# Optimization experiments

Measured on AMD Instinct MI355X. Metric: run time of the kernel, lower is better.

## Reference

```python
import jax, jax.numpy as jnp
import numpy as np

N = 50000; E = 1600000; F_IN = 32; HEADS = 8; D = 16; HID = HEADS * D
ED = 16; G = 512; MH = 512; MO = 512; SLOPE = 0.2


def setup_inputs() -> dict:
    key = jax.random.key(0)
    ks = jax.random.split(key, 40)
    inp = {}
    inp["x"] = jax.random.normal(ks[0], (N, F_IN), jnp.float32)
    inp["edge_index"] = jax.random.randint(ks[1], (2, E), 0, N)
    inp["edge_attr"] = jax.random.normal(ks[2], (E, ED), jnp.float32)
    inp["batch"] = jnp.sort(jax.random.randint(ks[3], (N,), 0, G))

    def lin(k, fi, fo):
        return jax.random.normal(k, (fi, fo), jnp.float32) / np.sqrt(fi).astype(np.float32)

    i = 4
    dims = [(F_IN, HID), (HID, HID), (HID, HID)]  # GATv2 layers 0..2
    for l, (fi, fo) in enumerate(dims):
        inp[f"Wl{l}"] = lin(ks[i], fi, fo); i += 1
        inp[f"bl{l}"] = jnp.zeros((fo,), jnp.float32)
        inp[f"Wr{l}"] = lin(ks[i], fi, fo); i += 1
        inp[f"br{l}"] = jnp.zeros((fo,), jnp.float32)
        inp[f"We{l}"] = lin(ks[i], ED, fo); i += 1
        inp[f"att{l}"] = jax.random.normal(ks[i], (HEADS, D), jnp.float32) / np.sqrt(D).astype(np.float32); i += 1
        inp[f"b{l}"] = jnp.zeros((fo,), jnp.float32)
    inp["mW1"] = lin(ks[i], HID, MH); i += 1
    inp["mb1"] = jnp.zeros((MH,), jnp.float32)
    inp["ln_g"] = jnp.ones((MH,), jnp.float32)
    inp["ln_b"] = jnp.zeros((MH,), jnp.float32)
    inp["mW2"] = lin(ks[i], MH, MO); i += 1
    inp["mb2"] = jnp.zeros((MO,), jnp.float32)
    return inp


def _gatv2(h, src, dst, ea, Wl, bl, Wr, br, We, att, b):
    # One GATv2Conv layer (eval mode, add_self_loops already applied).
    n = h.shape[0]
    xl = (h @ Wl + bl).reshape(n, HEADS, D)   # source transform
    xr = (h @ Wr + br).reshape(n, HEADS, D)   # target transform
    ee = (ea @ We).reshape(-1, HEADS, D)      # edge transform (no bias in PyG)
    m = xl[src] + xr[dst] + ee                # [E', H, D]
    m = jnp.where(m > 0, m, SLOPE * m)        # LeakyReLU(0.2)
    s = jnp.einsum('ehd,hd->eh', m, att)      # attention logits
    mx = jax.ops.segment_max(s, dst, num_segments=n)
    ex = jnp.exp(s - mx[dst])
    den = jax.ops.segment_sum(ex, dst, num_segments=n)
    alpha = ex / den[dst]                     # softmax over incoming edges
    out = jax.ops.segment_sum(alpha[:, :, None] * xl[src], dst, num_segments=n)
    return out.reshape(n, HEADS * D) + b


def _forward(x, edge_index, edge_attr, batch,
             Wl0, bl0, Wr0, br0, We0, att0, b0,
             Wl1, bl1, Wr1, br1, We1, att1, b1,
             Wl2, bl2, Wr2, br2, We2, att2, b2,
             mW1, mb1, ln_g, ln_b, mW2, mb2):
    src, dst = edge_index[0], edge_index[1]
    # add_self_loops with fill_value='mean': self-loop edge_attr = mean of incoming edge_attr
    cnt = jax.ops.segment_sum(jnp.ones((E,), jnp.float32), dst, num_segments=N)
    loop_attr = jax.ops.segment_sum(edge_attr, dst, num_segments=N) / jnp.clip(cnt, 1.0)[:, None]
    nodes = jnp.arange(N)
    src_f = jnp.concatenate([src, nodes])
    dst_f = jnp.concatenate([dst, nodes])
    ea = jnp.concatenate([edge_attr, loop_attr], axis=0)

    h = jax.nn.relu(_gatv2(x, src_f, dst_f, ea, Wl0, bl0, Wr0, br0, We0, att0, b0))
    h = jax.nn.relu(_gatv2(h, src_f, dst_f, ea, Wl1, bl1, Wr1, br1, We1, att1, b1))
    h = _gatv2(h, src_f, dst_f, ea, Wl2, bl2, Wr2, br2, We2, att2, b2)

    g = jax.ops.segment_sum(h, batch, num_segments=G)  # sum pooling per graph
    z = jax.nn.relu(g @ mW1 + mb1)
    mu = jnp.mean(z, axis=-1, keepdims=True)
    var = jnp.var(z, axis=-1, keepdims=True)
    z = (z - mu) / jnp.sqrt(var + 1e-5) * ln_g + ln_b
    return z @ mW2 + mb2


def reference(x, edge_index, edge_attr, batch,
              Wl0, bl0, Wr0, br0, We0, att0, b0,
              Wl1, bl1, Wr1, br1, We1, att1, b1,
              Wl2, bl2, Wr2, br2, We2, att2, b2,
              mW1, mb1, ln_g, ln_b, mW2, mb2):
    return _forward(x, edge_index, edge_attr, batch,
                    Wl0, bl0, Wr0, br0, We0, att0, b0,
                    Wl1, bl1, Wr1, br1, We1, att1, b1,
                    Wl2, bl2, Wr2, br2, We2, att2, b2,
                    mW1, mb1, ln_g, ln_b, mW2, mb2)
```

## Files before the change

### kernel.cpp

```cpp
#include <hip/hip_runtime.h>
#include <math.h>

#define NN 50000
#define EE 1600000
#define FIN 32
#define HID_ 128
#define ED_ 16
#define GG 512
#define MH_ 512
#define MO_ 512

#if __has_builtin(__builtin_amdgcn_exp2f)
#define EXP2(x) __builtin_amdgcn_exp2f(x)
#else
#define EXP2(x) exp2f(x)
#endif


__global__ void hist_kernel(const int* __restrict__ dst, int* __restrict__ cnt) {
  int e = blockIdx.x * 256 + threadIdx.x;
  if (e < EE) atomicAdd(&cnt[dst[e]], 1);
}

__global__ __launch_bounds__(256) void scan1_kernel(const int* __restrict__ in, int n,
                                                    int* __restrict__ out,
                                                    int* __restrict__ bsums) {
  int chunk = blockIdx.x;
  int base = chunk * 1024;
  int t = threadIdx.x;
  int idx = base + t * 4;
  int v0 = (idx + 0 < n) ? in[idx + 0] : 0;
  int v1 = (idx + 1 < n) ? in[idx + 1] : 0;
  int v2 = (idx + 2 < n) ? in[idx + 2] : 0;
  int v3 = (idx + 3 < n) ? in[idx + 3] : 0;
  int ts = v0 + v1 + v2 + v3;
  int lane = t & 63, w = t >> 6;
  int s = ts;
#pragma unroll
  for (int off = 1; off < 64; off <<= 1) {
    int o = __shfl_up(s, off);
    if (lane >= off) s += o;
  }
  __shared__ int wsum[4];
  if (lane == 63) wsum[w] = s;
  __syncthreads();
  int woff = 0;
  for (int i = 0; i < w; i++) woff += wsum[i];
  int excl = woff + s - ts;
  int run = excl;
  run += v0; if (idx + 0 < n) out[idx + 0] = run;
  run += v1; if (idx + 1 < n) out[idx + 1] = run;
  run += v2; if (idx + 2 < n) out[idx + 2] = run;
  run += v3; if (idx + 3 < n) out[idx + 3] = run;
  if (t == 255) bsums[chunk] = woff + s;
}

__global__ void scan_add_kernel(int* __restrict__ rowptr, const int* __restrict__ bscan, int n) {
  int i = blockIdx.x * 256 + threadIdx.x;
  if (i == 0) rowptr[0] = 0;
  if (i < n) {
    int chunk = i >> 10;
    if (chunk > 0) rowptr[1 + i] += bscan[chunk - 1];
  }
}

__global__ void scatter_kernel(const int* __restrict__ src, const int* __restrict__ dst,
                               const int* __restrict__ rowptr, int* __restrict__ fill,
                               int2* __restrict__ csr) {
  int e = blockIdx.x * 256 + threadIdx.x;
  if (e >= EE) return;
  int v = dst[e];
  int pos = rowptr[v] + atomicAdd(&fill[v], 1);
  csr[pos] = make_int2(src[e], e);
}

__global__ __launch_bounds__(256) void loopattr_kernel(const int* __restrict__ rowptr,
                                                       const int2* __restrict__ csr,
                                                       const float* __restrict__ ea,
                                                       float* __restrict__ la) {
  int wid = threadIdx.x >> 6, lane = threadIdx.x & 63;
  int v = __builtin_amdgcn_readfirstlane(blockIdx.x * 4 + wid);
  if (v >= NN) return;
  int s = __builtin_amdgcn_readfirstlane(rowptr[v]);
  int e = __builtin_amdgcn_readfirstlane(rowptr[v + 1]);
  int k = lane >> 4;
  int d = lane & 15;
  float acc = 0.f;
  for (int j = s + k; j < e; j += 4) acc += ea[(size_t)csr[j].y * 16 + d];
  acc += __shfl_xor(acc, 16);
  acc += __shfl_xor(acc, 32);
  if (lane < 16) la[(size_t)v * 16 + d] = (e > s) ? acc / (float)(e - s) : 0.f;
}


template <int F>
__global__ __launch_bounds__(256) void node_transform(const float* __restrict__ h,
                                                      const float* __restrict__ Wlm,
                                                      const float* __restrict__ blm,
                                                      const float* __restrict__ Wrm,
                                                      const float* __restrict__ brm,
                                                      float* __restrict__ xl,
                                                      float* __restrict__ xr, int nnodes) {
  __shared__ float hs[F * 32];
  int v0 = blockIdx.x * 32;
  int t = threadIdx.x;
  for (int idx = t; idx < 32 * F; idx += 256) {
    int i = idx / F, k = idx - i * F;
    float val = (v0 + i < nnodes) ? h[(size_t)(v0 + i) * F + k] : 0.f;
    hs[k * 32 + i] = val;
  }
  __syncthreads();
  int cc = t & 127;
  bool isL = t < 128;
  const float* W = isL ? Wlm : Wrm;
  float4 acc[8];
#pragma unroll
  for (int q = 0; q < 8; q++) acc[q] = make_float4(0.f, 0.f, 0.f, 0.f);
  const float4* hs4 = (const float4*)hs;
  for (int k = 0; k < F; k++) {
    float w = W[k * 128 + cc];
#pragma unroll
    for (int q = 0; q < 8; q++) {
      float4 hv = hs4[k * 8 + q];
      acc[q].x = fmaf(hv.x, w, acc[q].x);
      acc[q].y = fmaf(hv.y, w, acc[q].y);
      acc[q].z = fmaf(hv.z, w, acc[q].z);
      acc[q].w = fmaf(hv.w, w, acc[q].w);
    }
  }
  float b = isL ? blm[cc] : brm[cc];
  float* dstp = isL ? xl : xr;
  int nb = nnodes - v0; if (nb > 32) nb = 32;
#pragma unroll
  for (int q = 0; q < 8; q++) {
    if (4 * q + 0 < nb) dstp[(size_t)(v0 + 4 * q + 0) * 128 + cc] = acc[q].x + b;
    if (4 * q + 1 < nb) dstp[(size_t)(v0 + 4 * q + 1) * 128 + cc] = acc[q].y + b;
    if (4 * q + 2 < nb) dstp[(size_t)(v0 + 4 * q + 2) * 128 + cc] = acc[q].z + b;
    if (4 * q + 3 < nb) dstp[(size_t)(v0 + 4 * q + 3) * 128 + cc] = acc[q].w + b;
  }
}


__global__ __launch_bounds__(256) void gat_aggregate(
    const float* __restrict__ xl, const float* __restrict__ xr,
    const int* __restrict__ rowptr, const int2* __restrict__ csr,
    const float* __restrict__ ea, const float* __restrict__ la,
    const float* __restrict__ We, const float* __restrict__ att,
    const float* __restrict__ bias, float* __restrict__ hout, int relu) {
  int wid = threadIdx.x >> 6, lane = threadIdx.x & 63;
  int v = __builtin_amdgcn_readfirstlane(blockIdx.x * 4 + wid);
  if (v >= NN) return;
  int c0 = lane, c1 = 64 + lane;
  float wec0[16], wec1[16];
#pragma unroll
  for (int k = 0; k < 16; k++) {
    wec0[k] = We[k * 128 + c0];
    wec1[k] = We[k * 128 + c1];
  }
  const float L2E = 1.44269504088896340736f;
  float a0 = att[c0] * L2E, a1 = att[c1] * L2E;
  float xr0 = xr[(size_t)v * 128 + c0], xr1 = xr[(size_t)v * 128 + c1];

  auto score = [&](int u, const float* eaP,
                   float& xlu0, float& xlu1, float& p0, float& p1) {
    float ec[16];
#pragma unroll
    for (int k = 0; k < 4; k++) {
      float4 q = ((const float4*)eaP)[k];
      ec[4 * k + 0] = q.x; ec[4 * k + 1] = q.y;
      ec[4 * k + 2] = q.z; ec[4 * k + 3] = q.w;
    }
    const float* xlu = xl + (size_t)u * 128;
    xlu0 = xlu[c0]; xlu1 = xlu[c1];
    float m0 = xr0 + xlu0, m1 = xr1 + xlu1;
#pragma unroll
    for (int k = 0; k < 16; k++) {
      m0 = fmaf(ec[k], wec0[k], m0);
      m1 = fmaf(ec[k], wec1[k], m1);
    }
    m0 = fmaxf(m0, 0.2f * m0);
    m1 = fmaxf(m1, 0.2f * m1);
    p0 = a0 * m0; p1 = a1 * m1;
#pragma unroll
    for (int off = 1; off < 16; off <<= 1) {
      p0 += __shfl_xor(p0, off);
      p1 += __shfl_xor(p1, off);
    }
  };

  float mx0, mx1, den0 = 1.f, den1 = 1.f, acc0, acc1;
  {
    float xs0, xs1, p0, p1;
    score(v, la + (size_t)v * 16, xs0, xs1, p0, p1);
    mx0 = p0; mx1 = p1; acc0 = xs0; acc1 = xs1;
  }
  int start = __builtin_amdgcn_readfirstlane(rowptr[v]);
  int end = __builtin_amdgcn_readfirstlane(rowptr[v + 1]);
  int j = start;
  for (; j + 1 < end; j += 2) {
    int2 ep0 = csr[j], ep1 = csr[j + 1];
    float xa0, xa1, pa0, pa1, xb0, xb1, pb0, pb1;
    score(ep0.x, ea + (size_t)ep0.y * 16, xa0, xa1, pa0, pa1);
    score(ep1.x, ea + (size_t)ep1.y * 16, xb0, xb1, pb0, pb1);
    float nm0 = fmaxf(mx0, fmaxf(pa0, pb0));
    float f0 = EXP2(mx0 - nm0), wa0 = EXP2(pa0 - nm0), wb0 = EXP2(pb0 - nm0);
    den0 = fmaf(den0, f0, wa0 + wb0);
    acc0 = fmaf(acc0, f0, fmaf(wa0, xa0, wb0 * xb0));
    mx0 = nm0;
    float nm1 = fmaxf(mx1, fmaxf(pa1, pb1));
    float f1 = EXP2(mx1 - nm1), wa1 = EXP2(pa1 - nm1), wb1 = EXP2(pb1 - nm1);
    den1 = fmaf(den1, f1, wa1 + wb1);
    acc1 = fmaf(acc1, f1, fmaf(wa1, xa1, wb1 * xb1));
    mx1 = nm1;
  }
  if (j < end) {
    int2 ep0 = csr[j];
    float xa0, xa1, pa0, pa1;
    score(ep0.x, ea + (size_t)ep0.y * 16, xa0, xa1, pa0, pa1);
    float nm0 = fmaxf(mx0, pa0);
    float f0 = EXP2(mx0 - nm0), wa0 = EXP2(pa0 - nm0);
    den0 = fmaf(den0, f0, wa0);
    acc0 = fmaf(acc0, f0, wa0 * xa0);
    float nm1 = fmaxf(mx1, pa1);
    float f1 = EXP2(mx1 - nm1), wa1 = EXP2(pa1 - nm1);
    den1 = fmaf(den1, f1, wa1);
    acc1 = fmaf(acc1, f1, wa1 * xa1);
  }
  float o0 = acc0 / den0 + bias[c0];
  float o1 = acc1 / den1 + bias[c1];
  if (relu) { o0 = fmaxf(o0, 0.f); o1 = fmaxf(o1, 0.f); }
  hout[(size_t)v * 128 + c0] = o0;
  hout[(size_t)v * 128 + c1] = o1;
}


__global__ void gptr_kernel(const int* __restrict__ batch, int* __restrict__ gptr) {
  int g = blockIdx.x * 256 + threadIdx.x;
  if (g > GG) return;
  int lo = 0, hi = NN;
  while (lo < hi) {
    int mid = (lo + hi) >> 1;
    if (batch[mid] < g) lo = mid + 1; else hi = mid;
  }
  gptr[g] = lo;
}

__global__ void pool_kernel(const float* __restrict__ h, const int* __restrict__ gptr,
                            float* __restrict__ gp) {
  int gi = blockIdx.x;
  int c = threadIdx.x;
  int s = gptr[gi], e = gptr[gi + 1];
  float acc = 0.f;
  for (int v = s; v < e; v++) acc += h[(size_t)v * 128 + c];
  gp[gi * 128 + c] = acc;
}

__global__ __launch_bounds__(256) void mlp1_kernel(const float* __restrict__ gp,
                                                   const float* __restrict__ mW1,
                                                   const float* __restrict__ mb1,
                                                   const float* __restrict__ lng,
                                                   const float* __restrict__ lnb,
                                                   float* __restrict__ z) {
  int row = blockIdx.x;
  int t = threadIdx.x;
  __shared__ float gs[128];
  if (t < 128) gs[t] = gp[row * 128 + t];
  __syncthreads();
  int c0 = t, c1 = t + 256;
  float z0 = 0.f, z1 = 0.f;
  for (int k = 0; k < 128; k++) {
    float gk = gs[k];
    z0 = fmaf(gk, mW1[k * 512 + c0], z0);
    z1 = fmaf(gk, mW1[k * 512 + c1], z1);
  }
  z0 += mb1[c0]; z1 += mb1[c1];
  z0 = fmaxf(z0, 0.f); z1 = fmaxf(z1, 0.f);
  float s = z0 + z1, q = z0 * z0 + z1 * z1;
#pragma unroll
  for (int off = 32; off > 0; off >>= 1) {
    s += __shfl_xor(s, off);
    q += __shfl_xor(q, off);
  }
  __shared__ float red[8];
  int lane = t & 63, w = t >> 6;
  if (lane == 0) { red[w] = s; red[4 + w] = q; }
  __syncthreads();
  float S = red[0] + red[1] + red[2] + red[3];
  float Q = red[4] + red[5] + red[6] + red[7];
  float mu = S / 512.f;
  float var = Q / 512.f - mu * mu;
  float inv = 1.f / sqrtf(var + 1e-5f);
  z[row * 512 + c0] = (z0 - mu) * inv * lng[c0] + lnb[c0];
  z[row * 512 + c1] = (z1 - mu) * inv * lng[c1] + lnb[c1];
}

__global__ __launch_bounds__(256) void mlp2_kernel(const float* __restrict__ z,
                                                   const float* __restrict__ mW2,
                                                   const float* __restrict__ mb2,
                                                   float* __restrict__ out) {
  int row = blockIdx.x;
  int t = threadIdx.x;
  __shared__ float zs[512];
  for (int i = t; i < 512; i += 256) zs[i] = z[row * 512 + i];
  __syncthreads();
  int c0 = t, c1 = t + 256;
  float o0 = 0.f, o1 = 0.f;
  for (int k = 0; k < 512; k++) {
    float zk = zs[k];
    o0 = fmaf(zk, mW2[k * 512 + c0], o0);
    o1 = fmaf(zk, mW2[k * 512 + c1], o1);
  }
  out[row * 512 + c0] = o0 + mb2[c0];
  out[row * 512 + c1] = o1 + mb2[c1];
}


extern "C" void kernel_launch(void* const* d_in, const int* in_sizes, int n_in,
                              void* d_out, int out_size, void* d_ws, size_t ws_size,
                              hipStream_t stream) {
  const float* x = (const float*)d_in[0];
  const int* ei = (const int*)d_in[1];
  const int* srcE = ei;
  const int* dstE = ei + EE;
  const float* ea = (const float*)d_in[2];
  const int* batch = (const int*)d_in[3];
  const float* Wl[3] = {(const float*)d_in[4], (const float*)d_in[11], (const float*)d_in[18]};
  const float* bl[3] = {(const float*)d_in[5], (const float*)d_in[12], (const float*)d_in[19]};
  const float* Wr[3] = {(const float*)d_in[6], (const float*)d_in[13], (const float*)d_in[20]};
  const float* br[3] = {(const float*)d_in[7], (const float*)d_in[14], (const float*)d_in[21]};
  const float* Wek[3] = {(const float*)d_in[8], (const float*)d_in[15], (const float*)d_in[22]};
  const float* attk[3] = {(const float*)d_in[9], (const float*)d_in[16], (const float*)d_in[23]};
  const float* bk[3] = {(const float*)d_in[10], (const float*)d_in[17], (const float*)d_in[24]};
  const float* mW1 = (const float*)d_in[25];
  const float* mb1 = (const float*)d_in[26];
  const float* lng = (const float*)d_in[27];
  const float* lnb = (const float*)d_in[28];
  const float* mW2 = (const float*)d_in[29];
  const float* mb2 = (const float*)d_in[30];
  float* outp = (float*)d_out;

  char* W = (char*)d_ws;
  size_t off = 0;
  auto take = [&](size_t b) -> void* {
    void* p = W + off;
    off += (b + 255) & ~(size_t)255;
    return p;
  };
  int* cnt = (int*)take(NN * 4);
  int* rowptr = (int*)take((NN + 1) * 4);
  int* bsums = (int*)take(64 * 4);
  int* bscan = (int*)take(64 * 4);
  int* dummy = (int*)take(64 * 4);
  int2* csr = (int2*)take((size_t)EE * 8);
  float* la = (float*)take((size_t)NN * 16 * 4);
  float* xl = (float*)take((size_t)NN * HID_ * 4);
  float* xr = (float*)take((size_t)NN * HID_ * 4);
  float* hbuf = (float*)take((size_t)NN * HID_ * 4);
  int* gptr = (int*)take((GG + 1) * 4);
  float* gpool = (float*)take((size_t)GG * HID_ * 4);
  float* z = (float*)take((size_t)GG * MH_ * 4);
  (void)ws_size; (void)n_in; (void)in_sizes; (void)out_size;

  hipMemsetAsync(cnt, 0, NN * 4, stream);
  hist_kernel<<<(EE + 255) / 256, 256, 0, stream>>>(dstE, cnt);
  scan1_kernel<<<49, 256, 0, stream>>>(cnt, NN, rowptr + 1, bsums);
  scan1_kernel<<<1, 256, 0, stream>>>(bsums, 49, bscan, dummy);
  scan_add_kernel<<<(NN + 255) / 256, 256, 0, stream>>>(rowptr, bscan, NN);
  hipMemsetAsync(cnt, 0, NN * 4, stream);
  scatter_kernel<<<(EE + 255) / 256, 256, 0, stream>>>(srcE, dstE, rowptr, cnt, csr);
  loopattr_kernel<<<(NN + 3) / 4, 256, 0, stream>>>(rowptr, csr, ea, la);

  for (int l = 0; l < 3; l++) {
    if (l == 0)
      node_transform<FIN><<<(NN + 31) / 32, 256, 0, stream>>>(x, Wl[0], bl[0], Wr[0], br[0],
                                                              xl, xr, NN);
    else
      node_transform<HID_><<<(NN + 31) / 32, 256, 0, stream>>>(hbuf, Wl[l], bl[l], Wr[l], br[l],
                                                               xl, xr, NN);
    gat_aggregate<<<(NN + 3) / 4, 256, 0, stream>>>(xl, xr, rowptr, csr, ea, la,
                                                    Wek[l], attk[l], bk[l], hbuf,
                                                    (l < 2) ? 1 : 0);
  }

  gptr_kernel<<<3, 256, 0, stream>>>(batch, gptr);
  pool_kernel<<<GG, 128, 0, stream>>>(hbuf, gptr, gpool);
  mlp1_kernel<<<GG, 256, 0, stream>>>(gpool, mW1, mb1, lng, lnb, z);
  mlp2_kernel<<<GG, 256, 0, stream>>>(z, mW2, mb2, outp);
}
```

Before: 1.018 ms.

## Permute edge attributes into CSR order and vectorize GAT aggregation with lazy rescale

Adds a pass that copies edge attributes into CSR order so each aggregation reads them contiguously instead of gathering by edge id, used whenever the workspace has room. The aggregation kernel is rewritten to use packed two-float vector math and ds_swizzle butterfly reductions, and processes four edges per iteration with scalarized source indices. The online-softmax rescale exp is skipped when no lane's max increases. This costs an extra 100MB buffer and one permutation pass, and the uniform branch adds divergence checks.

```diff
diff --git a/kernel.cpp b/kernel.cpp
--- a/kernel.cpp
+++ b/kernel.cpp
@@ -10,11 +10,25 @@
 #define MH_ 512
 #define MO_ 512
 
+typedef float v2f __attribute__((ext_vector_type(2)));
+
 #if __has_builtin(__builtin_amdgcn_exp2f)
 #define EXP2(x) __builtin_amdgcn_exp2f(x)
 #else
 #define EXP2(x) exp2f(x)
 #endif
+
+__device__ __forceinline__ v2f exp2v(v2f a) {
+  v2f r; r.x = EXP2(a.x); r.y = EXP2(a.y); return r;
+}
+
+__device__ __forceinline__ float bfly16(float p) {
+  p += __uint_as_float(__builtin_amdgcn_ds_swizzle(__float_as_uint(p), 0x041F));
+  p += __uint_as_float(__builtin_amdgcn_ds_swizzle(__float_as_uint(p), 0x081F));
+  p += __uint_as_float(__builtin_amdgcn_ds_swizzle(__float_as_uint(p), 0x101F));
+  p += __uint_as_float(__builtin_amdgcn_ds_swizzle(__float_as_uint(p), 0x201F));
+  return p;
+}
 
 
 __global__ void hist_kernel(const int* __restrict__ dst, int* __restrict__ cnt) {
@@ -72,6 +86,15 @@
   int v = dst[e];
   int pos = rowptr[v] + atomicAdd(&fill[v], 1);
   csr[pos] = make_int2(src[e], e);
+}
+
+__global__ void permute_ea(const int2* __restrict__ csr, const float* __restrict__ ea,
+                           float* __restrict__ ea_csr) {
+  int t = blockIdx.x * 256 + threadIdx.x;
+  int j = t >> 2, q = t & 3;
+  if (j >= EE) return;
+  int eid = csr[j].y;
+  ((float4*)ea_csr)[t] = ((const float4*)ea)[eid * 4 + q];
 }
 
 __global__ __launch_bounds__(256) void loopattr_kernel(const int* __restrict__ rowptr,
@@ -141,28 +164,27 @@
 }
 
 
+template <bool PERM>
 __global__ __launch_bounds__(256) void gat_aggregate(
     const float* __restrict__ xl, const float* __restrict__ xr,
     const int* __restrict__ rowptr, const int2* __restrict__ csr,
-    const float* __restrict__ ea, const float* __restrict__ la,
+    const float* __restrict__ eaJ, const float* __restrict__ la,
     const float* __restrict__ We, const float* __restrict__ att,
     const float* __restrict__ bias, float* __restrict__ hout, int relu) {
   int wid = threadIdx.x >> 6, lane = threadIdx.x & 63;
   int v = __builtin_amdgcn_readfirstlane(blockIdx.x * 4 + wid);
   if (v >= NN) return;
-  int c0 = lane, c1 = 64 + lane;
-  float wec0[16], wec1[16];
+  v2f wec[16];
 #pragma unroll
   for (int k = 0; k < 16; k++) {
-    wec0[k] = We[k * 128 + c0];
-    wec1[k] = We[k * 128 + c1];
+    wec[k].x = We[k * 128 + lane];
+    wec[k].y = We[k * 128 + 64 + lane];
   }
   const float L2E = 1.44269504088896340736f;
-  float a0 = att[c0] * L2E, a1 = att[c1] * L2E;
-  float xr0 = xr[(size_t)v * 128 + c0], xr1 = xr[(size_t)v * 128 + c1];
-
-  auto score = [&](int u, const float* eaP,
-                   float& xlu0, float& xlu1, float& p0, float& p1) {
+  v2f av; av.x = att[lane] * L2E; av.y = att[64 + lane] * L2E;
+  v2f xrv; xrv.x = xr[(size_t)v * 128 + lane]; xrv.y = xr[(size_t)v * 128 + 64 + lane];
+
+  auto score = [&](int u, const float* eaP, v2f& xu, v2f& p) {
     float ec[16];
 #pragma unroll
     for (int k = 0; k < 4; k++) {
@@ -171,66 +193,95 @@
       ec[4 * k + 2] = q.z; ec[4 * k + 3] = q.w;
     }
     const float* xlu = xl + (size_t)u * 128;
-    xlu0 = xlu[c0]; xlu1 = xlu[c1];
-    float m0 = xr0 + xlu0, m1 = xr1 + xlu1;
+    xu.x = xlu[lane]; xu.y = xlu[64 + lane];
+    v2f m = xrv + xu;
 #pragma unroll
     for (int k = 0; k < 16; k++) {
-      m0 = fmaf(ec[k], wec0[k], m0);
-      m1 = fmaf(ec[k], wec1[k], m1);
-    }
-    m0 = fmaxf(m0, 0.2f * m0);
-    m1 = fmaxf(m1, 0.2f * m1);
-    p0 = a0 * m0; p1 = a1 * m1;
-#pragma unroll
-    for (int off = 1; off < 16; off <<= 1) {
-      p0 += __shfl_xor(p0, off);
-      p1 += __shfl_xor(p1, off);
-    }
+      v2f e2; e2.x = ec[k]; e2.y = ec[k];
+      m = __builtin_elementwise_fma(e2, wec[k], m);
+    }
+    m = __builtin_elementwise_max(m, 0.2f * m);
+    v2f q = av * m;
+    p.x = bfly16(q.x);
+    p.y = bfly16(q.y);
   };
 
-  float mx0, mx1, den0 = 1.f, den1 = 1.f, acc0, acc1;
+  v2f mx, den, acc;
   {
-    float xs0, xs1, p0, p1;
-    score(v, la + (size_t)v * 16, xs0, xs1, p0, p1);
-    mx0 = p0; mx1 = p1; acc0 = xs0; acc1 = xs1;
+    v2f xs, ps;
+    score(v, la + (size_t)v * 16, xs, ps);
+    mx = ps; den.x = 1.f; den.y = 1.f; acc = xs;
   }
   int start = __builtin_amdgcn_readfirstlane(rowptr[v]);
   int end = __builtin_amdgcn_readfirstlane(rowptr[v + 1]);
   int j = start;
-  for (; j + 1 < end; j += 2) {
-    int2 ep0 = csr[j], ep1 = csr[j + 1];
-    float xa0, xa1, pa0, pa1, xb0, xb1, pb0, pb1;
-    score(ep0.x, ea + (size_t)ep0.y * 16, xa0, xa1, pa0, pa1);
-    score(ep1.x, ea + (size_t)ep1.y * 16, xb0, xb1, pb0, pb1);
-    float nm0 = fmaxf(mx0, fmaxf(pa0, pb0));
-    float f0 = EXP2(mx0 - nm0), wa0 = EXP2(pa0 - nm0), wb0 = EXP2(pb0 - nm0);
-    den0 = fmaf(den0, f0, wa0 + wb0);
-    acc0 = fmaf(acc0, f0, fmaf(wa0, xa0, wb0 * xb0));
-    mx0 = nm0;
-    float nm1 = fmaxf(mx1, fmaxf(pa1, pb1));
-    float f1 = EXP2(mx1 - nm1), wa1 = EXP2(pa1 - nm1), wb1 = EXP2(pb1 - nm1);
-    den1 = fmaf(den1, f1, wa1 + wb1);
-    acc1 = fmaf(acc1, f1, fmaf(wa1, xa1, wb1 * xb1));
-    mx1 = nm1;
-  }
-  if (j < end) {
-    int2 ep0 = csr[j];
-    float xa0, xa1, pa0, pa1;
-    score(ep0.x, ea + (size_t)ep0.y * 16, xa0, xa1, pa0, pa1);
-    float nm0 = fmaxf(mx0, pa0);
-    float f0 = EXP2(mx0 - nm0), wa0 = EXP2(pa0 - nm0);
-    den0 = fmaf(den0, f0, wa0);
-    acc0 = fmaf(acc0, f0, wa0 * xa0);
-    float nm1 = fmaxf(mx1, pa1);
-    float f1 = EXP2(mx1 - nm1), wa1 = EXP2(pa1 - nm1);
-    den1 = fmaf(den1, f1, wa1);
-    acc1 = fmaf(acc1, f1, wa1 * xa1);
-  }
-  float o0 = acc0 / den0 + bias[c0];
-  float o1 = acc1 / den1 + bias[c1];
-  if (relu) { o0 = fmaxf(o0, 0.f); o1 = fmaxf(o1, 0.f); }
-  hout[(size_t)v * 128 + c0] = o0;
-  hout[(size_t)v * 128 + c1] = o1;
+  for (; j + 4 <= end; j += 4) {
+    int2 e0 = csr[j], e1 = csr[j + 1], e2 = csr[j + 2], e3 = csr[j + 3];
+    int u0 = __builtin_amdgcn_readfirstlane(e0.x);
+    int u1 = __builtin_amdgcn_readfirstlane(e1.x);
+    int u2 = __builtin_amdgcn_readfirstlane(e2.x);
+    int u3 = __builtin_amdgcn_readfirstlane(e3.x);
+    v2f xa, pa, xb, pb, xc, pc, xd, pd;
+    if (PERM) {
+      const float* b = eaJ + (size_t)j * 16;
+      score(u0, b, xa, pa);
+      score(u1, b + 16, xb, pb);
+      score(u2, b + 32, xc, pc);
+      score(u3, b + 48, xd, pd);
+    } else {
+      score(u0, eaJ + (size_t)e0.y * 16, xa, pa);
+      score(u1, eaJ + (size_t)e1.y * 16, xb, pb);
+      score(u2, eaJ + (size_t)e2.y * 16, xc, pc);
+      score(u3, eaJ + (size_t)e3.y * 16, xd, pd);
+    }
+    v2f pm = __builtin_elementwise_max(__builtin_elementwise_max(pa, pb),
+                                       __builtin_elementwise_max(pc, pd));
+    bool up = (pm.x > mx.x) || (pm.y > mx.y);
+    if (__any(up)) {
+      v2f nm = __builtin_elementwise_max(mx, pm);
+      v2f f = exp2v(mx - nm);
+      v2f wa = exp2v(pa - nm), wb = exp2v(pb - nm);
+      v2f wc = exp2v(pc - nm), wd = exp2v(pd - nm);
+      den = __builtin_elementwise_fma(f, den, (wa + wb) + (wc + wd));
+      v2f wx = __builtin_elementwise_fma(wa, xa,
+               __builtin_elementwise_fma(wb, xb,
+               __builtin_elementwise_fma(wc, xc, wd * xd)));
+      acc = __builtin_elementwise_fma(f, acc, wx);
+      mx = nm;
+    } else {
+      v2f wa = exp2v(pa - mx), wb = exp2v(pb - mx);
+      v2f wc = exp2v(pc - mx), wd = exp2v(pd - mx);
+      den += (wa + wb) + (wc + wd);
+      acc = __builtin_elementwise_fma(wa, xa,
+            __builtin_elementwise_fma(wb, xb,
+            __builtin_elementwise_fma(wc, xc,
+            __builtin_elementwise_fma(wd, xd, acc))));
+    }
+  }
+  for (; j < end; ++j) {
+    int2 e0 = csr[j];
+    int u0 = __builtin_amdgcn_readfirstlane(e0.x);
+    v2f xa, pa;
+    score(u0, PERM ? eaJ + (size_t)j * 16 : eaJ + (size_t)e0.y * 16, xa, pa);
+    bool up = (pa.x > mx.x) || (pa.y > mx.y);
+    if (__any(up)) {
+      v2f nm = __builtin_elementwise_max(mx, pa);
+      v2f f = exp2v(mx - nm);
+      v2f wa = exp2v(pa - nm);
+      den = __builtin_elementwise_fma(f, den, wa);
+      acc = __builtin_elementwise_fma(f, acc, wa * xa);
+      mx = nm;
+    } else {
+      v2f wa = exp2v(pa - mx);
+      den += wa;
+      acc = __builtin_elementwise_fma(wa, xa, acc);
+    }
+  }
+  v2f o = acc / den;
+  o.x += bias[lane]; o.y += bias[64 + lane];
+  if (relu) { o.x = fmaxf(o.x, 0.f); o.y = fmaxf(o.y, 0.f); }
+  hout[(size_t)v * 128 + lane] = o.x;
+  hout[(size_t)v * 128 + 64 + lane] = o.y;
 }
 
 
@@ -359,7 +410,9 @@
   int* gptr = (int*)take((GG + 1) * 4);
   float* gpool = (float*)take((size_t)GG * HID_ * 4);
   float* z = (float*)take((size_t)GG * MH_ * 4);
-  (void)ws_size; (void)n_in; (void)in_sizes; (void)out_size;
+  float* ea_csr = (float*)take((size_t)EE * 16 * 4);
+  bool perm = (off <= ws_size);
+  (void)n_in; (void)in_sizes; (void)out_size;
 
   hipMemsetAsync(cnt, 0, NN * 4, stream);
   hist_kernel<<<(EE + 255) / 256, 256, 0, stream>>>(dstE, cnt);
@@ -368,6 +421,8 @@
   scan_add_kernel<<<(NN + 255) / 256, 256, 0, stream>>>(rowptr, bscan, NN);
   hipMemsetAsync(cnt, 0, NN * 4, stream);
   scatter_kernel<<<(EE + 255) / 256, 256, 0, stream>>>(srcE, dstE, rowptr, cnt, csr);
+  if (perm)
+    permute_ea<<<(EE * 4 + 255) / 256, 256, 0, stream>>>(csr, ea, ea_csr);
   loopattr_kernel<<<(NN + 3) / 4, 256, 0, stream>>>(rowptr, csr, ea, la);
 
   for (int l = 0; l < 3; l++) {
@@ -377,9 +432,14 @@
     else
       node_transform<HID_><<<(NN + 31) / 32, 256, 0, stream>>>(hbuf, Wl[l], bl[l], Wr[l], br[l],
                                                                xl, xr, NN);
-    gat_aggregate<<<(NN + 3) / 4, 256, 0, stream>>>(xl, xr, rowptr, csr, ea, la,
-                                                    Wek[l], attk[l], bk[l], hbuf,
-                                                    (l < 2) ? 1 : 0);
+    if (perm)
+      gat_aggregate<true><<<(NN + 3) / 4, 256, 0, stream>>>(xl, xr, rowptr, csr, ea_csr, la,
+                                                            Wek[l], attk[l], bk[l], hbuf,
+                                                            (l < 2) ? 1 : 0);
+    else
+      gat_aggregate<false><<<(NN + 3) / 4, 256, 0, stream>>>(xl, xr, rowptr, csr, ea, la,
+                                                             Wek[l], attk[l], bk[l], hbuf,
+                                                             (l < 2) ? 1 : 0);
   }
 
   gptr_kernel<<<3, 256, 0, stream>>>(batch, gptr);
```

Result: slower. 1.090 ms (+7.1%).

## Permute edge attributes into CSR order and simplify GAT aggregation with packed math

Applied to the files above, without the earlier changes.

The scatter pass now also copies each edge's 16 attributes into destination-sorted CSR order, stored in extra workspace. The aggregation and self-loop-attribute kernels can then read edge attributes contiguously instead of gathering them by edge id. The CSR index array is split into separate src and eid arrays. The aggregation kernel maps two adjacent channels per lane with packed v2f FMAs, reduces heads over 8 lanes via ds_swizzle, and drops the online-max softmax rescaling, accumulating plain exp2 weights. The node transform is also rewritten to use packed v2f math. Costs and risks: an extra 100MB permutation write in scatter, a fallback path when the workspace is too small, and possible overflow, since softmax logits are no longer max-shifted.

```diff
diff --git a/kernel.cpp b/kernel.cpp
--- a/kernel.cpp
+++ b/kernel.cpp
@@ -10,11 +10,20 @@
 #define MH_ 512
 #define MO_ 512
 
+typedef float v2f __attribute__((ext_vector_type(2)));
+
 #if __has_builtin(__builtin_amdgcn_exp2f)
 #define EXP2(x) __builtin_amdgcn_exp2f(x)
 #else
 #define EXP2(x) exp2f(x)
 #endif
+
+__device__ __forceinline__ float bfly8(float p) {
+  p += __uint_as_float(__builtin_amdgcn_ds_swizzle(__float_as_uint(p), 0x041F));
+  p += __uint_as_float(__builtin_amdgcn_ds_swizzle(__float_as_uint(p), 0x081F));
+  p += __uint_as_float(__builtin_amdgcn_ds_swizzle(__float_as_uint(p), 0x101F));
+  return p;
+}
 
 
 __global__ void hist_kernel(const int* __restrict__ dst, int* __restrict__ cnt) {
@@ -64,19 +73,31 @@
   }
 }
 
+template <bool PERM>
 __global__ void scatter_kernel(const int* __restrict__ src, const int* __restrict__ dst,
                                const int* __restrict__ rowptr, int* __restrict__ fill,
-                               int2* __restrict__ csr) {
+                               int* __restrict__ csr_src, int* __restrict__ csr_eid,
+                               const float4* __restrict__ ea4, float4* __restrict__ ea_csr4) {
   int e = blockIdx.x * 256 + threadIdx.x;
   if (e >= EE) return;
   int v = dst[e];
   int pos = rowptr[v] + atomicAdd(&fill[v], 1);
-  csr[pos] = make_int2(src[e], e);
-}
-
+  csr_src[pos] = src[e];
+  csr_eid[pos] = e;
+  if (PERM) {
+    float4 a = ea4[e * 4 + 0], b = ea4[e * 4 + 1];
+    float4 c = ea4[e * 4 + 2], d = ea4[e * 4 + 3];
+    ea_csr4[(size_t)pos * 4 + 0] = a;
+    ea_csr4[(size_t)pos * 4 + 1] = b;
+    ea_csr4[(size_t)pos * 4 + 2] = c;
+    ea_csr4[(size_t)pos * 4 + 3] = d;
+  }
+}
+
+template <bool PERM>
 __global__ __launch_bounds__(256) void loopattr_kernel(const int* __restrict__ rowptr,
-                                                       const int2* __restrict__ csr,
-                                                       const float* __restrict__ ea,
+                                                       const int* __restrict__ csr_eid,
+                                                       const float* __restrict__ eaX,
                                                        float* __restrict__ la) {
   int wid = threadIdx.x >> 6, lane = threadIdx.x & 63;
   int v = __builtin_amdgcn_readfirstlane(blockIdx.x * 4 + wid);
@@ -86,7 +107,11 @@
   int k = lane >> 4;
   int d = lane & 15;
   float acc = 0.f;
-  for (int j = s + k; j < e; j += 4) acc += ea[(size_t)csr[j].y * 16 + d];
+  if (PERM) {
+    for (int j = s + k; j < e; j += 4) acc += eaX[(size_t)j * 16 + d];
+  } else {
+    for (int j = s + k; j < e; j += 4) acc += eaX[(size_t)csr_eid[j] * 16 + d];
+  }
   acc += __shfl_xor(acc, 16);
   acc += __shfl_xor(acc, 32);
   if (lane < 16) la[(size_t)v * 16 + d] = (e > s) ? acc / (float)(e - s) : 0.f;
@@ -106,131 +131,98 @@
   int t = threadIdx.x;
   for (int idx = t; idx < 32 * F; idx += 256) {
     int i = idx / F, k = idx - i * F;
-    float val = (v0 + i < nnodes) ? h[(size_t)(v0 + i) * F + k] : 0.f;
-    hs[k * 32 + i] = val;
-  }
-  __syncthreads();
-  int cc = t & 127;
+    hs[k * 32 + i] = (v0 + i < nnodes) ? h[(size_t)(v0 + i) * F + k] : 0.f;
+  }
+  __syncthreads();
   bool isL = t < 128;
-  const float* W = isL ? Wlm : Wrm;
-  float4 acc[8];
-#pragma unroll
-  for (int q = 0; q < 8; q++) acc[q] = make_float4(0.f, 0.f, 0.f, 0.f);
-  const float4* hs4 = (const float4*)hs;
+  int q = t & 63;
+  int nh = (t >> 6) & 1;
+  const float* Wm = isL ? Wlm : Wrm;
+  v2f acc[16];
+#pragma unroll
+  for (int i = 0; i < 16; i++) acc[i] = (v2f){0.f, 0.f};
   for (int k = 0; k < F; k++) {
-    float w = W[k * 128 + cc];
-#pragma unroll
-    for (int q = 0; q < 8; q++) {
-      float4 hv = hs4[k * 8 + q];
-      acc[q].x = fmaf(hv.x, w, acc[q].x);
-      acc[q].y = fmaf(hv.y, w, acc[q].y);
-      acc[q].z = fmaf(hv.z, w, acc[q].z);
-      acc[q].w = fmaf(hv.w, w, acc[q].w);
+    v2f w = *(const v2f*)(Wm + k * 128 + 2 * q);
+    const float4* hk4 = (const float4*)(hs + k * 32 + nh * 16);
+#pragma unroll
+    for (int r = 0; r < 4; r++) {
+      float4 hv = hk4[r];
+      acc[4 * r + 0] = __builtin_elementwise_fma((v2f){hv.x, hv.x}, w, acc[4 * r + 0]);
+      acc[4 * r + 1] = __builtin_elementwise_fma((v2f){hv.y, hv.y}, w, acc[4 * r + 1]);
+      acc[4 * r + 2] = __builtin_elementwise_fma((v2f){hv.z, hv.z}, w, acc[4 * r + 2]);
+      acc[4 * r + 3] = __builtin_elementwise_fma((v2f){hv.w, hv.w}, w, acc[4 * r + 3]);
     }
   }
-  float b = isL ? blm[cc] : brm[cc];
+  const float* bm = isL ? blm : brm;
+  v2f b = *(const v2f*)(bm + 2 * q);
   float* dstp = isL ? xl : xr;
-  int nb = nnodes - v0; if (nb > 32) nb = 32;
-#pragma unroll
-  for (int q = 0; q < 8; q++) {
-    if (4 * q + 0 < nb) dstp[(size_t)(v0 + 4 * q + 0) * 128 + cc] = acc[q].x + b;
-    if (4 * q + 1 < nb) dstp[(size_t)(v0 + 4 * q + 1) * 128 + cc] = acc[q].y + b;
-    if (4 * q + 2 < nb) dstp[(size_t)(v0 + 4 * q + 2) * 128 + cc] = acc[q].z + b;
-    if (4 * q + 3 < nb) dstp[(size_t)(v0 + 4 * q + 3) * 128 + cc] = acc[q].w + b;
-  }
-}
-
-
+  int base = v0 + nh * 16;
+#pragma unroll
+  for (int i = 0; i < 16; i++) {
+    if (base + i < nnodes)
+      *(v2f*)(dstp + (size_t)(base + i) * 128 + 2 * q) = acc[i] + b;
+  }
+}
+
+
+template <bool PERM>
 __global__ __launch_bounds__(256) void gat_aggregate(
     const float* __restrict__ xl, const float* __restrict__ xr,
-    const int* __restrict__ rowptr, const int2* __restrict__ csr,
-    const float* __restrict__ ea, const float* __restrict__ la,
-    const float* __restrict__ We, const float* __restrict__ att,
-    const float* __restrict__ bias, float* __restrict__ hout, int relu) {
+    const int* __restrict__ rowptr, const int* __restrict__ csr_src,
+    const int* __restrict__ csr_eid, const float* __restrict__ eaJ,
+    const float* __restrict__ la, const float* __restrict__ We,
+    const float* __restrict__ att, const float* __restrict__ bias,
+    float* __restrict__ hout, int relu) {
   int wid = threadIdx.x >> 6, lane = threadIdx.x & 63;
   int v = __builtin_amdgcn_readfirstlane(blockIdx.x * 4 + wid);
   if (v >= NN) return;
-  int c0 = lane, c1 = 64 + lane;
-  float wec0[16], wec1[16];
-#pragma unroll
-  for (int k = 0; k < 16; k++) {
-    wec0[k] = We[k * 128 + c0];
-    wec1[k] = We[k * 128 + c1];
-  }
+  int c = 2 * lane;
+  v2f wec[16];
+#pragma unroll
+  for (int k = 0; k < 16; k++) wec[k] = *(const v2f*)(We + k * 128 + c);
   const float L2E = 1.44269504088896340736f;
-  float a0 = att[c0] * L2E, a1 = att[c1] * L2E;
-  float xr0 = xr[(size_t)v * 128 + c0], xr1 = xr[(size_t)v * 128 + c1];
-
-  auto score = [&](int u, const float* eaP,
-                   float& xlu0, float& xlu1, float& p0, float& p1) {
-    float ec[16];
-#pragma unroll
-    for (int k = 0; k < 4; k++) {
-      float4 q = ((const float4*)eaP)[k];
-      ec[4 * k + 0] = q.x; ec[4 * k + 1] = q.y;
-      ec[4 * k + 2] = q.z; ec[4 * k + 3] = q.w;
+  v2f av = *(const v2f*)(att + c) * L2E;
+  v2f xrv = *(const v2f*)(xr + (size_t)v * 128 + c);
+
+  auto score = [&](int u, const float* eaP, v2f& xu) -> float {
+    xu = *(const v2f*)(xl + (size_t)u * 128 + c);
+    v2f m = xrv + xu;
+#pragma unroll
+    for (int k = 0; k < 16; k++) {
+      float e = eaP[k];
+      m = __builtin_elementwise_fma((v2f){e, e}, wec[k], m);
     }
-    const float* xlu = xl + (size_t)u * 128;
-    xlu0 = xlu[c0]; xlu1 = xlu[c1];
-    float m0 = xr0 + xlu0, m1 = xr1 + xlu1;
-#pragma unroll
-    for (int k = 0; k < 16; k++) {
-      m0 = fmaf(ec[k], wec0[k], m0);
-      m1 = fmaf(ec[k], wec1[k], m1);
-    }
-    m0 = fmaxf(m0, 0.2f * m0);
-    m1 = fmaxf(m1, 0.2f * m1);
-    p0 = a0 * m0; p1 = a1 * m1;
-#pragma unroll
-    for (int off = 1; off < 16; off <<= 1) {
-      p0 += __shfl_xor(p0, off);
-      p1 += __shfl_xor(p1, off);
-    }
+    m = __builtin_elementwise_max(m, 0.2f * m);
+    v2f qq = av * m;
+    return bfly8(qq.x + qq.y);
   };
 
-  float mx0, mx1, den0 = 1.f, den1 = 1.f, acc0, acc1;
+  v2f acc;
+  float den;
   {
-    float xs0, xs1, p0, p1;
-    score(v, la + (size_t)v * 16, xs0, xs1, p0, p1);
-    mx0 = p0; mx1 = p1; acc0 = xs0; acc1 = xs1;
+    v2f xu;
+    float p = score(v, la + (size_t)v * 16, xu);
+    float w = EXP2(p);
+    den = w;
+    acc = (v2f){w, w} * xu;
   }
   int start = __builtin_amdgcn_readfirstlane(rowptr[v]);
   int end = __builtin_amdgcn_readfirstlane(rowptr[v + 1]);
-  int j = start;
-  for (; j + 1 < end; j += 2) {
-    int2 ep0 = csr[j], ep1 = csr[j + 1];
-    float xa0, xa1, pa0, pa1, xb0, xb1, pb0, pb1;
-    score(ep0.x, ea + (size_t)ep0.y * 16, xa0, xa1, pa0, pa1);
-    score(ep1.x, ea + (size_t)ep1.y * 16, xb0, xb1, pb0, pb1);
-    float nm0 = fmaxf(mx0, fmaxf(pa0, pb0));
-    float f0 = EXP2(mx0 - nm0), wa0 = EXP2(pa0 - nm0), wb0 = EXP2(pb0 - nm0);
-    den0 = fmaf(den0, f0, wa0 + wb0);
-    acc0 = fmaf(acc0, f0, fmaf(wa0, xa0, wb0 * xb0));
-    mx0 = nm0;
-    float nm1 = fmaxf(mx1, fmaxf(pa1, pb1));
-    float f1 = EXP2(mx1 - nm1), wa1 = EXP2(pa1 - nm1), wb1 = EXP2(pb1 - nm1);
-    den1 = fmaf(den1, f1, wa1 + wb1);
-    acc1 = fmaf(acc1, f1, fmaf(wa1, xa1, wb1 * xb1));
-    mx1 = nm1;
-  }
-  if (j < end) {
-    int2 ep0 = csr[j];
-    float xa0, xa1, pa0, pa1;
-    score(ep0.x, ea + (size_t)ep0.y * 16, xa0, xa1, pa0, pa1);
-    float nm0 = fmaxf(mx0, pa0);
-    float f0 = EXP2(mx0 - nm0), wa0 = EXP2(pa0 - nm0);
-    den0 = fmaf(den0, f0, wa0);
-    acc0 = fmaf(acc0, f0, wa0 * xa0);
-    float nm1 = fmaxf(mx1, pa1);
-    float f1 = EXP2(mx1 - nm1), wa1 = EXP2(pa1 - nm1);
-    den1 = fmaf(den1, f1, wa1);
-    acc1 = fmaf(acc1, f1, wa1 * xa1);
-  }
-  float o0 = acc0 / den0 + bias[c0];
-  float o1 = acc1 / den1 + bias[c1];
-  if (relu) { o0 = fmaxf(o0, 0.f); o1 = fmaxf(o1, 0.f); }
-  hout[(size_t)v * 128 + c0] = o0;
-  hout[(size_t)v * 128 + c1] = o1;
+  for (int j = start; j < end; ++j) {
+    int u = __builtin_amdgcn_readfirstlane(csr_src[j]);
+    const float* eaP = PERM ? eaJ + (size_t)j * 16
+                            : eaJ + (size_t)__builtin_amdgcn_readfirstlane(csr_eid[j]) * 16;
+    v2f xu;
+    float p = score(u, eaP, xu);
+    float w = EXP2(p);
+    den += w;
+    acc = __builtin_elementwise_fma((v2f){w, w}, xu, acc);
+  }
+  float invd = 1.f / den;
+  v2f bv = *(const v2f*)(bias + c);
+  v2f o = __builtin_elementwise_fma(acc, (v2f){invd, invd}, bv);
+  if (relu) o = __builtin_elementwise_max(o, (v2f){0.f, 0.f});
+  *(v2f*)(hout + (size_t)v * 128 + c) = o;
 }
 
 
@@ -351,7 +343,8 @@
   int* bsums = (int*)take(64 * 4);
   int* bscan = (int*)take(64 * 4);
   int* dummy = (int*)take(64 * 4);
-  int2* csr = (int2*)take((size_t)EE * 8);
+  int* csr_src = (int*)take((size_t)EE * 4);
+  int* csr_eid = (int*)take((size_t)EE * 4);
   float* la = (float*)take((size_t)NN * 16 * 4);
   float* xl = (float*)take((size_t)NN * HID_ * 4);
   float* xr = (float*)take((size_t)NN * HID_ * 4);
@@ -359,7 +352,9 @@
   int* gptr = (int*)take((GG + 1) * 4);
   float* gpool = (float*)take((size_t)GG * HID_ * 4);
   float* z = (float*)take((size_t)GG * MH_ * 4);
-  (void)ws_size; (void)n_in; (void)in_sizes; (void)out_size;
+  float* ea_csr = (float*)take((size_t)EE * 16 * 4);
+  bool perm = (off <= ws_size);
+  (void)n_in; (void)in_sizes; (void)out_size;
 
   hipMemsetAsync(cnt, 0, NN * 4, stream);
   hist_kernel<<<(EE + 255) / 256, 256, 0, stream>>>(dstE, cnt);
@@ -367,8 +362,15 @@
   scan1_kernel<<<1, 256, 0, stream>>>(bsums, 49, bscan, dummy);
   scan_add_kernel<<<(NN + 255) / 256, 256, 0, stream>>>(rowptr, bscan, NN);
   hipMemsetAsync(cnt, 0, NN * 4, stream);
-  scatter_kernel<<<(EE + 255) / 256, 256, 0, stream>>>(srcE, dstE, rowptr, cnt, csr);
-  loopattr_kernel<<<(NN + 3) / 4, 256, 0, stream>>>(rowptr, csr, ea, la);
+  if (perm) {
+    scatter_kernel<true><<<(EE + 255) / 256, 256, 0, stream>>>(
+        srcE, dstE, rowptr, cnt, csr_src, csr_eid, (const float4*)ea, (float4*)ea_csr);
+    loopattr_kernel<true><<<(NN + 3) / 4, 256, 0, stream>>>(rowptr, csr_eid, ea_csr, la);
+  } else {
+    scatter_kernel<false><<<(EE + 255) / 256, 256, 0, stream>>>(
+        srcE, dstE, rowptr, cnt, csr_src, csr_eid, (const float4*)ea, nullptr);
+    loopattr_kernel<false><<<(NN + 3) / 4, 256, 0, stream>>>(rowptr, csr_eid, ea, la);
+  }
 
   for (int l = 0; l < 3; l++) {
     if (l == 0)
@@ -377,9 +379,14 @@
     else
       node_transform<HID_><<<(NN + 31) / 32, 256, 0, stream>>>(hbuf, Wl[l], bl[l], Wr[l], br[l],
                                                                xl, xr, NN);
-    gat_aggregate<<<(NN + 3) / 4, 256, 0, stream>>>(xl, xr, rowptr, csr, ea, la,
-                                                    Wek[l], attk[l], bk[l], hbuf,
-                                                    (l < 2) ? 1 : 0);
+    if (perm)
+      gat_aggregate<true><<<(NN + 3) / 4, 256, 0, stream>>>(
+          xl, xr, rowptr, csr_src, csr_eid, ea_csr, la, Wek[l], attk[l], bk[l], hbuf,
+          (l < 2) ? 1 : 0);
+    else
+      gat_aggregate<false><<<(NN + 3) / 4, 256, 0, stream>>>(
+          xl, xr, rowptr, csr_src, csr_eid, ea, la, Wek[l], attk[l], bk[l], hbuf,
+          (l < 2) ? 1 : 0);
   }
 
   gptr_kernel<<<3, 256, 0, stream>>>(batch, gptr);
```

Measured after the change: 1.135 ms. 11.5% more time.
